# Kernel tuning notes

Hardware: AMD Instinct MI355X
Metric: run time of the kernel (lower is better)

Reference implementation:

```python
import jax, jax.numpy as jnp
import numpy as np

B, T, E, HSZ = 128, 256, 512, 1024
VOCAB, LVOCAB, K, STEPS = 2048, 11, 6, 3
HD = HSZ // 2  # per-direction LSTM hidden


def _lstm_dir(x, W_ih, W_hh, b, reverse):
    # x: [B,T,E] -> h seq [B,T,HD]; PyTorch gate order i,f,g,o
    xp = jnp.einsum('bte,ge->btg', x, W_ih) + b  # [B,T,4HD]
    if reverse:
        xp = xp[:, ::-1]
    def step(carry, xt):
        h, c = carry
        g = xt + h @ W_hh.T
        i, f, gg, o = jnp.split(g, 4, axis=-1)
        c = jax.nn.sigmoid(f) * c + jax.nn.sigmoid(i) * jnp.tanh(gg)
        h = jax.nn.sigmoid(o) * jnp.tanh(c)
        return (h, c), h
    z = jnp.zeros((x.shape[0], HD), x.dtype)
    _, hs = jax.lax.scan(step, (z, z), jnp.swapaxes(xp, 0, 1))
    hs = jnp.swapaxes(hs, 0, 1)
    if reverse:
        hs = hs[:, ::-1]
    return hs


def setup_inputs() -> dict:
    key = jax.random.key(0)
    ks = jax.random.split(key, 16)
    Xs = jax.random.randint(ks[0], (B, T), 0, VOCAB)
    seq_mask = jnp.ones((B, T), jnp.float32)
    landmarks = jax.random.randint(ks[1], (B, 4, 4, K), 0, LVOCAB)
    ys = jax.random.randint(ks[2], (B, 2), 0, 4)
    s = 0.05
    emb = (jax.random.normal(ks[3], (VOCAB, E)) * s).at[0].set(0.0)  # padding_idx=0
    W_ih_f = jax.random.normal(ks[4], (4 * HD, E)) * s
    W_hh_f = jax.random.normal(ks[5], (4 * HD, HD)) * s
    b_f = jax.random.normal(ks[6], (4 * HD,)) * s
    W_ih_b = jax.random.normal(ks[7], (4 * HD, E)) * s
    W_hh_b = jax.random.normal(ks[8], (4 * HD, HD)) * s
    b_b = jax.random.normal(ks[9], (4 * HD,)) * s
    feat_ctrl = jax.random.normal(ks[10], (HSZ,)) * 0.1
    upd_W = jax.random.normal(ks[11], (HSZ, 2 * HSZ)) * s
    upd_b = jax.random.normal(ks[12], (HSZ,)) * s
    map_emb = (jax.random.normal(ks[13], (LVOCAB, HSZ)) * s).at[0].set(0.0)
    std = 1.0 / (HSZ * 9)
    conv_w = jax.random.uniform(ks[14], (HSZ, HSZ, 3, 3), minval=-std, maxval=std)
    return dict(Xs=Xs, seq_mask=seq_mask, landmarks=landmarks, ys=ys, emb=emb,
                W_ih_f=W_ih_f, W_hh_f=W_hh_f, b_f=b_f, W_ih_b=W_ih_b,
                W_hh_b=W_hh_b, b_b=b_b, feat_ctrl=feat_ctrl, upd_W=upd_W,
                upd_b=upd_b, map_emb=map_emb, conv_w=conv_w)


def reference(Xs, seq_mask, landmarks, ys, emb, W_ih_f, W_hh_f, b_f,
              W_ih_b, W_hh_b, b_b, feat_ctrl, upd_W, upd_b, map_emb, conv_w):
    bsz = Xs.shape[0]
    x = emb[Xs]  # [B,T,E]
    hf = _lstm_dir(x, W_ih_f, W_hh_f, b_f, False)
    hb = _lstm_dir(x, W_ih_b, W_hh_b, b_b, True)
    hidden = jnp.concatenate([hf, hb], -1)  # [B,T,HSZ]

    controller = jnp.broadcast_to(feat_ctrl, (bsz, HSZ))
    msgs = []
    for _ in range(STEPS):
        score = jnp.einsum('bth,bh->bt', hidden, controller)
        score = score - 1e30 * (1.0 - seq_mask)
        att = jax.nn.softmax(score, axis=-1)
        msg = jnp.einsum('bt,bth->bh', att, hidden)
        msgs.append(msg)
        controller = jnp.concatenate([msg, controller], 1) @ upd_W.T + upd_b
    feature_msg = jnp.concatenate(msgs, 1)  # [B, STEPS*HSZ]

    # MapEmbedding2d: sum landmark embeddings per cell -> [B,4,4,HSZ] -> NCHW
    l_emb = map_emb[landmarks].sum(-2).transpose(0, 3, 1, 2)
    # masked conv weight: 4-neighbor diffusion
    m = jnp.zeros((3, 3)).at[0, 1].set(1.0).at[1, 0].set(1.0).at[2, 1].set(1.0).at[1, 2].set(1.0)
    w = conv_w * m[None, None]
    l_embs = [l_emb]
    for _ in range(STEPS - 1):
        l_embs.append(jax.lax.conv_general_dilated(
            l_embs[-1], w, (1, 1), [(1, 1), (1, 1)],
            dimension_numbers=('NCHW', 'OIHW', 'NCHW')))
    lmk = jnp.concatenate(l_embs, 1)  # [B, STEPS*HSZ, 4, 4]
    lmk = lmk.reshape(bsz, lmk.shape[1], 16).transpose(0, 2, 1)  # [B,16,C]
    logits = jnp.einsum('bnc,bc->bn', lmk, feature_msg)  # [B,16]
    prob = jax.nn.softmax(logits, 1)
    y_true = ys[:, 0] * 4 + ys[:, 1]
    # faithful to original: CrossEntropyLoss applied to prob (softmax of softmax)
    logp = jax.nn.log_softmax(prob, 1)
    loss = -jnp.take_along_axis(logp, y_true[:, None], 1).mean()
    acc = jnp.mean((jnp.argmax(prob, 1) == y_true).astype(jnp.float32))
    return loss, acc
```

## Files before the change

### kernel.cpp

```cpp
#include <hip/hip_runtime.h>


typedef _Float16 f16;
typedef __attribute__((ext_vector_type(8))) _Float16 f16x8;
typedef __attribute__((ext_vector_type(4))) float f32x4;

#define DEV __device__ __forceinline__

DEV void gload_lds16(const void* g, void* lds) {
  __builtin_amdgcn_global_load_lds(
      (const __attribute__((address_space(1))) unsigned*)g,
      (__attribute__((address_space(3))) unsigned*)lds, 16, 0, 0);
}
DEV void gload_lds16c(const void* g, void* lds) {
  __builtin_amdgcn_global_load_lds(
      (const __attribute__((address_space(1))) unsigned*)g,
      (__attribute__((address_space(3))) unsigned*)lds, 16, 0, 17);
}
DEV float sigm(float x) { return 1.0f / (1.0f + __expf(-x)); }
DEV float tanh_(float x) { return 1.0f - 2.0f / (__expf(2.0f * x) + 1.0f); }
DEV unsigned pck(float a, float b) {
  union { unsigned u; f16 h[2]; } c; c.h[0] = (f16)a; c.h[1] = (f16)b; return c.u;
}

__global__ __launch_bounds__(256) void gemm_kernel(
    const f16* __restrict__ A, const f16* __restrict__ B,
    const float* __restrict__ bias, void* __restrict__ Cp,
    int M, int N, int K, int cmode) {
  __shared__ f16 As[128 * 32];
  __shared__ f16 Bs[128 * 32];
  const int tid = threadIdx.x;
  const int w = tid >> 6, l = tid & 63;
  const int m0 = blockIdx.x * 128, n0 = blockIdx.y * 128;
  const int wm = (w & 1) * 64, wn = (w >> 1) * 64;
  const int lr = l & 15, lq = l >> 4;
  const int srow = w * 32 + (l >> 2);
  const int kc8 = (l & 3) * 8;
  f32x4 acc[4][4];
#pragma unroll
  for (int i = 0; i < 4; ++i)
#pragma unroll
    for (int j = 0; j < 4; ++j) acc[i][j] = (f32x4){0.f, 0.f, 0.f, 0.f};

  for (int kt = 0; kt < K; kt += 32) {
    __syncthreads();
#pragma unroll
    for (int i = 0; i < 2; ++i) {
      gload_lds16(A + (long)(m0 + srow + i * 16) * K + kt + kc8,
                  &As[(w * 32 + i * 16) * 32]);
      gload_lds16(B + (long)(n0 + srow + i * 16) * K + kt + kc8,
                  &Bs[(w * 32 + i * 16) * 32]);
    }
    __syncthreads();
    f16x8 af[4], bf[4];
#pragma unroll
    for (int mi = 0; mi < 4; ++mi)
      af[mi] = *(const f16x8*)&As[(wm + mi * 16 + lr) * 32 + lq * 8];
#pragma unroll
    for (int ni = 0; ni < 4; ++ni)
      bf[ni] = *(const f16x8*)&Bs[(wn + ni * 16 + lr) * 32 + lq * 8];
#pragma unroll
    for (int mi = 0; mi < 4; ++mi)
#pragma unroll
      for (int ni = 0; ni < 4; ++ni)
        acc[mi][ni] =
            __builtin_amdgcn_mfma_f32_16x16x32_f16(af[mi], bf[ni], acc[mi][ni], 0, 0, 0);
  }
#pragma unroll
  for (int mi = 0; mi < 4; ++mi)
#pragma unroll
    for (int ni = 0; ni < 4; ++ni)
#pragma unroll
      for (int r = 0; r < 4; ++r) {
        const int m = m0 + wm + mi * 16 + lq * 4 + r;
        const int n = n0 + wn + ni * 16 + lr;
        float v = acc[mi][ni][r];
        if (bias) v += bias[n];
        if (cmode) ((f16*)Cp)[(long)m * N + n] = (f16)v;
        else       ((float*)Cp)[(long)m * N + n] = v;
      }
}

__global__ __launch_bounds__(256, 1) void lstm_kernel(
    const f16* __restrict__ x16,
    const float* __restrict__ Wih_f, const float* __restrict__ Wih_b,
    const float* __restrict__ Whh_f, const float* __restrict__ Whh_b,
    const float* __restrict__ b_f, const float* __restrict__ b_b,
    f16* __restrict__ hg, f16* __restrict__ hidden, int* __restrict__ bar) {
  __shared__ f16 hs[16 * 16 * 32];
  __shared__ f16 xs[2][16 * 16 * 32];
  __shared__ float gb[4][16][32];
  const int blk = blockIdx.x, tid = threadIdx.x;
  const int d = blk >> 7, rr = blk & 127;
  const int ug = rr & 15, bg = rr >> 4;
  const int b0 = bg * 16;
  const int w = tid >> 6, l = tid & 63;
  const int lr = l & 15, lq = l >> 4;
  const int u0 = ug * 32 + w * 8;
  const float* const Wih = d ? Wih_b : Wih_f;
  const float* const Whh = d ? Whh_b : Whh_f;
  const float* const bb = d ? b_b : b_f;
  int* const flagbase = &bar[((d << 3) + bg) << 4];

  f16x8 wih[16][2], whh[16][2];
#pragma unroll
  for (int kt = 0; kt < 16; ++kt)
#pragma unroll
    for (int nt = 0; nt < 2; ++nt) {
      const int n = nt * 16 + lr;
      const long row = (long)((n >> 3) * 512 + u0 + (n & 7));
      const float* pi = Wih + row * 512 + kt * 32 + lq * 8;
      const float* ph = Whh + row * 512 + kt * 32 + lq * 8;
      f16x8 va, vb;
#pragma unroll
      for (int j = 0; j < 8; ++j) { va[j] = (f16)pi[j]; vb[j] = (f16)ph[j]; }
      wih[kt][nt] = va; whh[kt][nt] = vb;
    }
  const int bl = l >> 2, jp = (l & 3) * 2;
  const int b_my = b0 + bl;
  const float bi0 = bb[u0 + jp],        bi1 = bb[u0 + jp + 1];
  const float bF0 = bb[512 + u0 + jp],  bF1 = bb[512 + u0 + jp + 1];
  const float bg0 = bb[1024 + u0 + jp], bg1 = bb[1024 + u0 + jp + 1];
  const float bo0 = bb[1536 + u0 + jp], bo1 = bb[1536 + u0 + jp + 1];
  float c0 = 0.f, c1 = 0.f;
  f16* const hbase = hg + (d * 2) * 65536;

#define STAGE16(DST, SRCP, LOADER)                                            \
  {                                                                           \
    const f16* _s = (SRCP);                                                   \
    _Pragma("unroll") for (int k4 = 0; k4 < 4; ++k4) {                        \
      const int kt = w * 4 + k4;                                              \
      LOADER(_s + (long)(l >> 2) * 512 + kt * 32 + (l & 3) * 8,               \
             &DST[(kt * 16) * 32]);                                           \
    }                                                                         \
  }

  STAGE16(xs[0], x16 + ((long)(d ? 255 : 0) * 128 + b0) * 512, gload_lds16);
  __builtin_amdgcn_s_waitcnt(0x0F70);
  __syncthreads();
  f32x4 a0 = (f32x4){0.f, 0.f, 0.f, 0.f}, a1 = (f32x4){0.f, 0.f, 0.f, 0.f};
#pragma unroll
  for (int kt = 0; kt < 16; ++kt) {
    const f16x8 av = *(const f16x8*)&xs[0][(kt * 16 + lr) * 32 + lq * 8];
    a0 = __builtin_amdgcn_mfma_f32_16x16x32_f16(av, wih[kt][0], a0, 0, 0, 0);
    a1 = __builtin_amdgcn_mfma_f32_16x16x32_f16(av, wih[kt][1], a1, 0, 0, 0);
  }
  STAGE16(xs[1], x16 + ((long)(d ? 254 : 1) * 128 + b0) * 512, gload_lds16);

  for (int s = 0; s < 256; ++s) {
    const int t = d ? (255 - s) : s;
    const f16* const hrd = hbase + (s & 1) * 65536;
    f16* const hwr = hbase + ((s + 1) & 1) * 65536;
    if (w == 0 && l < 16) {
      while (__hip_atomic_load(&flagbase[l], __ATOMIC_RELAXED,
                               __HIP_MEMORY_SCOPE_SYSTEM) < s)
        __builtin_amdgcn_s_sleep(1);
    }
    __syncthreads();
    STAGE16(hs, hrd + (long)b0 * 512, gload_lds16c);
    __builtin_amdgcn_s_waitcnt(0x0F70);
    __syncthreads();
#pragma unroll
    for (int kt = 0; kt < 16; ++kt) {
      const f16x8 av = *(const f16x8*)&hs[(kt * 16 + lr) * 32 + lq * 8];
      a0 = __builtin_amdgcn_mfma_f32_16x16x32_f16(av, whh[kt][0], a0, 0, 0, 0);
      a1 = __builtin_amdgcn_mfma_f32_16x16x32_f16(av, whh[kt][1], a1, 0, 0, 0);
    }
#pragma unroll
    for (int r = 0; r < 4; ++r) {
      gb[w][lq * 4 + r][lr] = a0[r];
      gb[w][lq * 4 + r][16 + lr] = a1[r];
    }
    __builtin_amdgcn_s_waitcnt(0xC07F);
    unsigned hp;
    {
      const float* const gr = &gb[w][bl][0];
      float gi = gr[jp] + bi0, gf = gr[8 + jp] + bF0;
      float gg = gr[16 + jp] + bg0, go = gr[24 + jp] + bo0;
      c0 = sigm(gf) * c0 + sigm(gi) * tanh_(gg);
      const float h0 = sigm(go) * tanh_(c0);
      gi = gr[jp + 1] + bi1; gf = gr[8 + jp + 1] + bF1;
      gg = gr[16 + jp + 1] + bg1; go = gr[24 + jp + 1] + bo1;
      c1 = sigm(gf) * c1 + sigm(gi) * tanh_(gg);
      const float h1 = sigm(go) * tanh_(c1);
      hp = pck(h0, h1);
      __hip_atomic_store((unsigned*)&hwr[(b_my << 9) + u0 + jp], hp,
                         __ATOMIC_RELAXED, __HIP_MEMORY_SCOPE_SYSTEM);
    }
    __builtin_amdgcn_s_waitcnt(0x0F70);
    __syncthreads();
    if (tid == 0)
      __hip_atomic_store(&flagbase[ug], s + 1, __ATOMIC_RELAXED,
                         __HIP_MEMORY_SCOPE_SYSTEM);
    *(unsigned*)&hidden[((long)b_my * 256 + t) * 1024 + (d << 9) + u0 + jp] = hp;
    if (s < 255) {
      a0 = (f32x4){0.f, 0.f, 0.f, 0.f}; a1 = (f32x4){0.f, 0.f, 0.f, 0.f};
      const f16* const xr = &xs[(s + 1) & 1][0];
#pragma unroll
      for (int kt = 0; kt < 16; ++kt) {
        const f16x8 av = *(const f16x8*)&xr[(kt * 16 + lr) * 32 + lq * 8];
        a0 = __builtin_amdgcn_mfma_f32_16x16x32_f16(av, wih[kt][0], a0, 0, 0, 0);
        a1 = __builtin_amdgcn_mfma_f32_16x16x32_f16(av, wih[kt][1], a1, 0, 0, 0);
      }
      if (s < 254) {
        const int tp = d ? (253 - s) : (s + 2);
        STAGE16(xs[s & 1], x16 + ((long)tp * 128 + b0) * 512, gload_lds16);
      }
    }
  }
#undef STAGE16
}

__global__ __launch_bounds__(256) void att_kernel(
    const f16* __restrict__ hidden, const float* __restrict__ ctrl,
    const float* __restrict__ seq_mask, float* __restrict__ msg_out,
    f16* __restrict__ cat) {
  __shared__ float sc[256];
  __shared__ float red[4];
  __shared__ float ctl[1024];
  const int b = blockIdx.x, tid = threadIdx.x;
  const int w = tid >> 6, l = tid & 63;
  for (int i = tid; i < 1024; i += 256) ctl[i] = ctrl[b * 1024 + i];
  __syncthreads();
  float cl[16];
#pragma unroll
  for (int j = 0; j < 16; ++j) cl[j] = ctl[l + 64 * j];
  const f16* hb = hidden + (long)b * 262144;
  for (int t = w * 64; t < w * 64 + 64; ++t) {
    float s = 0.f;
#pragma unroll
    for (int j = 0; j < 16; ++j) s += (float)hb[t * 1024 + l + 64 * j] * cl[j];
#pragma unroll
    for (int off = 32; off; off >>= 1) s += __shfl_xor(s, off);
    if (l == 0) sc[t] = s;
  }
  __syncthreads();
  const float v = sc[tid] - 1e30f * (1.0f - seq_mask[b * 256 + tid]);
  float m = v;
#pragma unroll
  for (int off = 32; off; off >>= 1) m = fmaxf(m, __shfl_xor(m, off));
  if (l == 0) red[w] = m;
  __syncthreads();
  const float M = fmaxf(fmaxf(red[0], red[1]), fmaxf(red[2], red[3]));
  const float e = __expf(v - M);
  float ss = e;
#pragma unroll
  for (int off = 32; off; off >>= 1) ss += __shfl_xor(ss, off);
  __syncthreads();
  if (l == 0) red[w] = ss;
  __syncthreads();
  const float S = red[0] + red[1] + red[2] + red[3];
  sc[tid] = e / S;
  __syncthreads();
  const int hc = tid * 4;
  float a0 = 0.f, a1 = 0.f, a2 = 0.f, a3 = 0.f;
  for (int t = 0; t < 256; ++t) {
    const float at = sc[t];
    union { uint2 u; f16 h[4]; } q;
    q.u = *(const uint2*)&hb[t * 1024 + hc];
    a0 += at * (float)q.h[0]; a1 += at * (float)q.h[1];
    a2 += at * (float)q.h[2]; a3 += at * (float)q.h[3];
  }
  float* mo = msg_out + b * 1024 + hc;
  mo[0] = a0; mo[1] = a1; mo[2] = a2; mo[3] = a3;
  if (cat) {
    f16* cm = cat + (long)b * 2048 + hc;
    cm[0] = (f16)a0; cm[1] = (f16)a1; cm[2] = (f16)a2; cm[3] = (f16)a3;
    f16* cc = cat + (long)b * 2048 + 1024 + hc;
    cc[0] = (f16)ctl[hc]; cc[1] = (f16)ctl[hc + 1];
    cc[2] = (f16)ctl[hc + 2]; cc[3] = (f16)ctl[hc + 3];
  }
}

__global__ __launch_bounds__(256) void l0_kernel(
    const int* __restrict__ lm, const float* __restrict__ me, f16* __restrict__ l0) {
  const int bp = blockIdx.x, tid = threadIdx.x;
  const int h = tid * 4;
  int id[6];
#pragma unroll
  for (int k = 0; k < 6; ++k) id[k] = lm[bp * 6 + k];
  float a0 = 0.f, a1 = 0.f, a2 = 0.f, a3 = 0.f;
#pragma unroll
  for (int k = 0; k < 6; ++k) {
    const float* r = me + id[k] * 1024 + h;
    a0 += r[0]; a1 += r[1]; a2 += r[2]; a3 += r[3];
  }
  union { uint2 u; f16 hh[4]; } pk;
  pk.hh[0] = (f16)a0; pk.hh[1] = (f16)a1; pk.hh[2] = (f16)a2; pk.hh[3] = (f16)a3;
  *(uint2*)&l0[(long)bp * 1024 + h] = pk.u;
}

__global__ __launch_bounds__(256) void patch_kernel(
    const f16* __restrict__ src, f16* __restrict__ patch) {
  const int bp = blockIdx.x, tid = threadIdx.x;
  const int b = bp >> 4, p = bp & 15, y = p >> 2, x = p & 3;
  const int base = b * 16;
  f16* pr = patch + (long)bp * 4096;
  for (int i = tid; i < 1024; i += 256) {
    union { uint2 u; f16 h[4]; } pk;
    pk.h[0] = (y > 0) ? src[(long)(base + p - 4) * 1024 + i] : (f16)0.f;
    pk.h[1] = (x > 0) ? src[(long)(base + p - 1) * 1024 + i] : (f16)0.f;
    pk.h[2] = (x < 3) ? src[(long)(base + p + 1) * 1024 + i] : (f16)0.f;
    pk.h[3] = (y < 3) ? src[(long)(base + p + 4) * 1024 + i] : (f16)0.f;
    *(uint2*)&pr[i * 4] = pk.u;
  }
}

__global__ __launch_bounds__(256) void logits_kernel(
    const f16* __restrict__ l0, const f16* __restrict__ l1, const f16* __restrict__ l2,
    const float* __restrict__ msgs, const int* __restrict__ ys, float* __restrict__ la) {
  __shared__ float lg[16];
  const int b = blockIdx.x, tid = threadIdx.x;
  const int p = tid >> 4, q = tid & 15;
  const float* m0 = msgs + b * 1024;
  const float* m1 = msgs + 131072 + b * 1024;
  const float* m2 = msgs + 262144 + b * 1024;
  const long row = (long)(b * 16 + p) * 1024;
  float part = 0.f;
  for (int i = 0; i < 64; ++i) {
    const int h = q + 16 * i;
    part += (float)l0[row + h] * m0[h] + (float)l1[row + h] * m1[h] +
            (float)l2[row + h] * m2[h];
  }
#pragma unroll
  for (int off = 8; off; off >>= 1) part += __shfl_xor(part, off, 16);
  if (q == 0) lg[p] = part;
  __syncthreads();
  if (tid == 0) {
    float mx = lg[0];
    for (int i = 1; i < 16; ++i) mx = fmaxf(mx, lg[i]);
    float pr[16]; float s = 0.f;
    for (int i = 0; i < 16; ++i) { pr[i] = __expf(lg[i] - mx); s += pr[i]; }
    for (int i = 0; i < 16; ++i) pr[i] /= s;
    float mx2 = pr[0];
    for (int i = 1; i < 16; ++i) mx2 = fmaxf(mx2, pr[i]);
    float s2 = 0.f;
    for (int i = 0; i < 16; ++i) s2 += __expf(pr[i] - mx2);
    const float lse = mx2 + __logf(s2);
    const int y = ys[b * 2] * 4 + ys[b * 2 + 1];
    const float logp = pr[y] - lse;
    int am = 0; float bv = pr[0];
    for (int i = 1; i < 16; ++i) if (pr[i] > bv) { bv = pr[i]; am = i; }
    atomicAdd(&la[0], -logp * (1.0f / 128.0f));
    atomicAdd(&la[1], (am == y) ? (1.0f / 128.0f) : 0.0f);
  }
}

__global__ void finalize_kernel(const float* __restrict__ la,
                                float* __restrict__ out) {
  if (threadIdx.x == 0) { out[0] = la[0]; out[1] = la[1]; }
}

__global__ __launch_bounds__(256) void embed_kernel(
    const int* __restrict__ Xs, const float* __restrict__ emb, f16* __restrict__ x16) {
  const int m = blockIdx.x, tid = threadIdx.x;
  const int t = m >> 7, b = m & 127;
  const int v = Xs[b * 256 + t];
  const int e = tid * 2;
  const float2 f = *(const float2*)&emb[(long)v * 512 + e];
  *(unsigned*)&x16[(long)m * 512 + e] = pck(f.x, f.y);
}

__global__ __launch_bounds__(256) void prep2_kernel(
    const float* __restrict__ upd_W, const float* __restrict__ conv_w,
    f16* __restrict__ updW16, f16* __restrict__ w4) {
  const int idx = blockIdx.x * 256 + threadIdx.x;
  if (idx < 2097152) updW16[idx] = (f16)upd_W[idx];
  const int o = idx >> 12, r = idx & 4095, i = r >> 2, tp = r & 3;
  w4[idx] = (f16)conv_w[(long)(o * 1024 + i) * 9 + 1 + 2 * tp];
}

__global__ __launch_bounds__(256) void init_kernel(
    f16* __restrict__ hg, int* __restrict__ bar, float* __restrict__ la,
    float* __restrict__ ctrlA, const float* __restrict__ feat) {
  const int idx = blockIdx.x * 256 + threadIdx.x;
  ((unsigned*)hg)[idx] = 0u;
  ctrlA[idx] = feat[idx & 1023];
  if (idx < 256) bar[idx] = 0;
  if (idx < 2) la[idx] = 0.f;
}

__global__ void fail_kernel(float* out, int mb) {
  if (threadIdx.x == 0) { out[0] = 12344.0f; out[1] = (float)mb; }
}

extern "C" void kernel_launch(void* const* d_in, const int* in_sizes, int n_in,
                              void* d_out, int out_size, void* d_ws, size_t ws_size,
                              hipStream_t stream) {
  (void)in_sizes; (void)n_in; (void)out_size;
  const int*   Xs      = (const int*)d_in[0];
  const float* seqmask = (const float*)d_in[1];
  const int*   lm      = (const int*)d_in[2];
  const int*   ys      = (const int*)d_in[3];
  const float* emb     = (const float*)d_in[4];
  const float* W_ih_f  = (const float*)d_in[5];
  const float* W_hh_f  = (const float*)d_in[6];
  const float* b_f     = (const float*)d_in[7];
  const float* W_ih_b  = (const float*)d_in[8];
  const float* W_hh_b  = (const float*)d_in[9];
  const float* b_b     = (const float*)d_in[10];
  const float* feat    = (const float*)d_in[11];
  const float* upd_W   = (const float*)d_in[12];
  const float* upd_b   = (const float*)d_in[13];
  const float* mapemb  = (const float*)d_in[14];
  const float* conv_w  = (const float*)d_in[15];
  float* out = (float*)d_out;
  char* ws = (char*)d_ws;
  size_t off = 0;
  auto alloc = [&](size_t bytes) {
    void* p = ws + off; off += (bytes + 255) & ~(size_t)255; return p;
  };
  f16*   x16    = (f16*)alloc(33554432);
  f16*   hid    = (f16*)alloc(67108864);
  f16*   hgb    = (f16*)alloc(524288);
  int*   bar    = (int*)alloc(1024);
  float* la     = (float*)alloc(256);
  float* ctrlA  = (float*)alloc(524288);
  float* ctrlB  = (float*)alloc(524288);
  float* msgs   = (float*)alloc(1572864);
  f16*   cat    = (f16*)alloc(524288);
  f16*   l0b    = (f16*)alloc(4194304);
  f16*   l1b    = (f16*)alloc(4194304);
  f16*   l2b    = (f16*)alloc(4194304);
  f16*   patch  = x16;
  f16*   w416   = x16 + 8388608;
  f16*   updW16 = x16 + 12582912;
  if (ws_size < off) {
    fail_kernel<<<1, 64, 0, stream>>>(out, (int)(off >> 20));
    return;
  }

  init_kernel<<<512, 256, 0, stream>>>(hgb, bar, la, ctrlA, feat);
  embed_kernel<<<32768, 256, 0, stream>>>(Xs, emb, x16);
  {
    void* args[] = {(void*)&x16, (void*)&W_ih_f, (void*)&W_ih_b,
                    (void*)&W_hh_f, (void*)&W_hh_b, (void*)&b_f, (void*)&b_b,
                    (void*)&hgb, (void*)&hid, (void*)&bar};
    hipLaunchCooperativeKernel((void*)lstm_kernel, dim3(256), dim3(256), args, 0, stream);
  }
  prep2_kernel<<<16384, 256, 0, stream>>>(upd_W, conv_w, updW16, w416);
  l0_kernel<<<2048, 256, 0, stream>>>(lm, mapemb, l0b);
  patch_kernel<<<2048, 256, 0, stream>>>(l0b, patch);
  gemm_kernel<<<dim3(16, 8), 256, 0, stream>>>(patch, w416, nullptr, l1b,
                                               2048, 1024, 4096, 1);
  patch_kernel<<<2048, 256, 0, stream>>>(l1b, patch);
  gemm_kernel<<<dim3(16, 8), 256, 0, stream>>>(patch, w416, nullptr, l2b,
                                               2048, 1024, 4096, 1);
  att_kernel<<<128, 256, 0, stream>>>(hid, ctrlA, seqmask, msgs, cat);
  gemm_kernel<<<dim3(1, 8), 256, 0, stream>>>(cat, updW16, upd_b, ctrlB,
                                              128, 1024, 2048, 0);
  att_kernel<<<128, 256, 0, stream>>>(hid, ctrlB, seqmask, msgs + 131072, cat);
  gemm_kernel<<<dim3(1, 8), 256, 0, stream>>>(cat, updW16, upd_b, ctrlA,
                                              128, 1024, 2048, 0);
  att_kernel<<<128, 256, 0, stream>>>(hid, ctrlA, seqmask, msgs + 262144, nullptr);
  logits_kernel<<<128, 256, 0, stream>>>(l0b, l1b, l2b, msgs, ys, la);
  finalize_kernel<<<1, 64, 0, stream>>>(la, out);
}
```

Baseline: 1.567 ms.

## Run landmark conv chain concurrently with LSTM in one cooperative mega-kernel

Merges the LSTM recurrence and the landmark embedding/conv pipeline into one cooperative launch. Blocks 0-255 run the LSTM while blocks 256+ compute l0 and both masked-conv GEMM steps, using an implicit-im2col conv tile so the patch kernels disappear. The LSTM now gathers embedding rows directly from an f16 embedding table rather than a precomputed x16 buffer, which removes the embed kernel's large write. Risks include contention for CUs and memory bandwidth with the latency-bound LSTM, and co-residency of 512 blocks with launch_bounds(256,2).

```diff
diff --git a/kernel.cpp b/kernel.cpp
--- a/kernel.cpp
+++ b/kernel.cpp
@@ -81,20 +81,126 @@
       }
 }
 
-__global__ __launch_bounds__(256, 1) void lstm_kernel(
-    const f16* __restrict__ x16,
+DEV void conv_tile(char* smem, int tid, const f16* lsrc, const f16* wsrc,
+                   f16* ldst, int m0, int n0, const f16* zbuf) {
+  f16* const As = (f16*)smem;
+  f16* const Bs = (f16*)(smem + 8192);
+  const int w = tid >> 6, l = tid & 63;
+  const int wm = (w & 1) * 64, wn = (w >> 1) * 64;
+  const int lr = l & 15, lq = l >> 4;
+  const int srow = w * 32 + (l >> 2);
+  const int kc8 = (l & 3) * 8;
+  f32x4 acc[4][4];
+#pragma unroll
+  for (int i = 0; i < 4; ++i)
+#pragma unroll
+    for (int j = 0; j < 4; ++j) acc[i][j] = (f32x4){0.f, 0.f, 0.f, 0.f};
+
+  for (int kt = 0; kt < 4096; kt += 32) {
+    __syncthreads();
+    const int k = kt + kc8, tap = k >> 10, ic = k & 1023;
+#pragma unroll
+    for (int i = 0; i < 2; ++i) {
+      const int m = m0 + srow + i * 16;
+      const int b = m >> 4, p = m & 15, py = p >> 2, px = p & 3;
+      const int nb = p + ((tap == 0) ? -4 : (tap == 1) ? -1 : (tap == 2) ? 1 : 4);
+      const bool ok = (tap == 0) ? (py > 0) : (tap == 1) ? (px > 0)
+                      : (tap == 2) ? (px < 3) : (py < 3);
+      const f16* sa = ok ? (lsrc + ((long)(b * 16 + nb) * 1024 + ic)) : zbuf;
+      gload_lds16(sa, &As[(w * 32 + i * 16) * 32]);
+      gload_lds16(wsrc + (long)(n0 + srow + i * 16) * 4096 + kt + kc8,
+                  &Bs[(w * 32 + i * 16) * 32]);
+    }
+    __syncthreads();
+    f16x8 af[4], bf[4];
+#pragma unroll
+    for (int mi = 0; mi < 4; ++mi)
+      af[mi] = *(const f16x8*)&As[(wm + mi * 16 + lr) * 32 + lq * 8];
+#pragma unroll
+    for (int ni = 0; ni < 4; ++ni)
+      bf[ni] = *(const f16x8*)&Bs[(wn + ni * 16 + lr) * 32 + lq * 8];
+#pragma unroll
+    for (int mi = 0; mi < 4; ++mi)
+#pragma unroll
+      for (int ni = 0; ni < 4; ++ni)
+        acc[mi][ni] =
+            __builtin_amdgcn_mfma_f32_16x16x32_f16(af[mi], bf[ni], acc[mi][ni], 0, 0, 0);
+  }
+#pragma unroll
+  for (int mi = 0; mi < 4; ++mi)
+#pragma unroll
+    for (int ni = 0; ni < 4; ++ni)
+#pragma unroll
+      for (int r = 0; r < 4; ++r) {
+        const int m = m0 + wm + mi * 16 + lq * 4 + r;
+        const int n = n0 + wn + ni * 16 + lr;
+        ldst[(long)m * 1024 + n] = (f16)acc[mi][ni][r];
+      }
+}
+
+DEV void helper_barrier(int* cnt, int* gen, int tid) {
+  __syncthreads();
+  if (tid == 0) {
+    __threadfence();
+    const int a = __hip_atomic_fetch_add(cnt, 1, __ATOMIC_ACQ_REL,
+                                         __HIP_MEMORY_SCOPE_SYSTEM);
+    if (a == 255) {
+      __hip_atomic_store(gen, 1, __ATOMIC_RELEASE, __HIP_MEMORY_SCOPE_SYSTEM);
+    } else {
+      while (__hip_atomic_load(gen, __ATOMIC_RELAXED,
+                               __HIP_MEMORY_SCOPE_SYSTEM) == 0)
+        __builtin_amdgcn_s_sleep(8);
+    }
+    __threadfence();
+  }
+  __syncthreads();
+}
+
+__global__ __launch_bounds__(256, 2) void mega_kernel(
+    const int* __restrict__ Xs, const f16* __restrict__ emb16,
     const float* __restrict__ Wih_f, const float* __restrict__ Wih_b,
     const float* __restrict__ Whh_f, const float* __restrict__ Whh_b,
     const float* __restrict__ b_f, const float* __restrict__ b_b,
-    f16* __restrict__ hg, f16* __restrict__ hidden, int* __restrict__ bar) {
-  __shared__ f16 hs[16 * 16 * 32];
-  __shared__ f16 xs[2][16 * 16 * 32];
-  __shared__ float gb[4][16][32];
+    f16* __restrict__ hg, f16* __restrict__ hidden, int* __restrict__ bar,
+    const int* __restrict__ lm, const float* __restrict__ mapemb,
+    f16* __restrict__ l0b, f16* __restrict__ l1b, f16* __restrict__ l2b,
+    const f16* __restrict__ w416, const f16* __restrict__ zbuf) {
+  __shared__ char smem[57344];
   const int blk = blockIdx.x, tid = threadIdx.x;
+  const int w = tid >> 6, l = tid & 63;
+
+  if (blk >= 256) {
+    const int hb = blk - 256;
+    for (int j = 0; j < 8; ++j) {
+      const int bp = hb * 8 + j;
+      const int h = tid * 4;
+      float a0 = 0.f, a1 = 0.f, a2 = 0.f, a3 = 0.f;
+#pragma unroll
+      for (int k = 0; k < 6; ++k) {
+        const float* r = mapemb + lm[bp * 6 + k] * 1024 + h;
+        a0 += r[0]; a1 += r[1]; a2 += r[2]; a3 += r[3];
+      }
+      union { uint2 u; f16 hh[4]; } pk;
+      pk.hh[0] = (f16)a0; pk.hh[1] = (f16)a1;
+      pk.hh[2] = (f16)a2; pk.hh[3] = (f16)a3;
+      *(uint2*)&l0b[(long)bp * 1024 + h] = pk.u;
+    }
+    helper_barrier(&bar[256], &bar[272], tid);
+    if (hb < 128)
+      conv_tile(smem, tid, l0b, w416, l1b, (hb & 15) * 128, (hb >> 4) * 128, zbuf);
+    helper_barrier(&bar[288], &bar[304], tid);
+    if (hb < 128)
+      conv_tile(smem, tid, l1b, w416, l2b, (hb & 15) * 128, (hb >> 4) * 128, zbuf);
+    return;
+  }
+
+  f16* const hs = (f16*)smem;
+  f16* const xs0 = (f16*)(smem + 16384);
+  f16* const xs1 = (f16*)(smem + 32768);
+  float* const gbp = (float*)(smem + 49152);
   const int d = blk >> 7, rr = blk & 127;
   const int ug = rr & 15, bg = rr >> 4;
   const int b0 = bg * 16;
-  const int w = tid >> 6, l = tid & 63;
   const int lr = l & 15, lq = l >> 4;
   const int u0 = ug * 32 + w * 8;
   const float* const Wih = d ? Wih_b : Wih_f;
@@ -125,27 +231,36 @@
   float c0 = 0.f, c1 = 0.f;
   f16* const hbase = hg + (d * 2) * 65536;
 
-#define STAGE16(DST, SRCP, LOADER)                                            \
+#define STAGEH(SRCP)                                                          \
   {                                                                           \
     const f16* _s = (SRCP);                                                   \
     _Pragma("unroll") for (int k4 = 0; k4 < 4; ++k4) {                        \
       const int kt = w * 4 + k4;                                              \
-      LOADER(_s + (long)(l >> 2) * 512 + kt * 32 + (l & 3) * 8,               \
-             &DST[(kt * 16) * 32]);                                           \
+      gload_lds16c(_s + (long)(l >> 2) * 512 + kt * 32 + (l & 3) * 8,         \
+                   &hs[(kt * 16) * 32]);                                      \
     }                                                                         \
   }
-
-  STAGE16(xs[0], x16 + ((long)(d ? 255 : 0) * 128 + b0) * 512, gload_lds16);
+#define STAGEX(DSTP, TP)                                                      \
+  {                                                                           \
+    const int _xr = Xs[(b0 + (l >> 2)) * 256 + (TP)];                         \
+    const f16* _s = emb16 + (long)_xr * 512 + (l & 3) * 8;                    \
+    _Pragma("unroll") for (int k4 = 0; k4 < 4; ++k4) {                        \
+      const int kt = w * 4 + k4;                                              \
+      gload_lds16(_s + kt * 32, &(DSTP)[(kt * 16) * 32]);                     \
+    }                                                                         \
+  }
+
+  STAGEX(xs0, d ? 255 : 0);
   __builtin_amdgcn_s_waitcnt(0x0F70);
   __syncthreads();
   f32x4 a0 = (f32x4){0.f, 0.f, 0.f, 0.f}, a1 = (f32x4){0.f, 0.f, 0.f, 0.f};
 #pragma unroll
   for (int kt = 0; kt < 16; ++kt) {
-    const f16x8 av = *(const f16x8*)&xs[0][(kt * 16 + lr) * 32 + lq * 8];
+    const f16x8 av = *(const f16x8*)&xs0[(kt * 16 + lr) * 32 + lq * 8];
     a0 = __builtin_amdgcn_mfma_f32_16x16x32_f16(av, wih[kt][0], a0, 0, 0, 0);
     a1 = __builtin_amdgcn_mfma_f32_16x16x32_f16(av, wih[kt][1], a1, 0, 0, 0);
   }
-  STAGE16(xs[1], x16 + ((long)(d ? 254 : 1) * 128 + b0) * 512, gload_lds16);
+  STAGEX(xs1, d ? 254 : 1);
 
   for (int s = 0; s < 256; ++s) {
     const int t = d ? (255 - s) : s;
@@ -157,7 +272,7 @@
         __builtin_amdgcn_s_sleep(1);
     }
     __syncthreads();
-    STAGE16(hs, hrd + (long)b0 * 512, gload_lds16c);
+    STAGEH(hrd + (long)b0 * 512);
     __builtin_amdgcn_s_waitcnt(0x0F70);
     __syncthreads();
 #pragma unroll
@@ -168,13 +283,13 @@
     }
 #pragma unroll
     for (int r = 0; r < 4; ++r) {
-      gb[w][lq * 4 + r][lr] = a0[r];
-      gb[w][lq * 4 + r][16 + lr] = a1[r];
+      gbp[(w * 16 + lq * 4 + r) * 32 + lr] = a0[r];
+      gbp[(w * 16 + lq * 4 + r) * 32 + 16 + lr] = a1[r];
     }
     __builtin_amdgcn_s_waitcnt(0xC07F);
     unsigned hp;
     {
-      const float* const gr = &gb[w][bl][0];
+      const float* const gr = &gbp[(w * 16 + bl) * 32];
       float gi = gr[jp] + bi0, gf = gr[8 + jp] + bF0;
       float gg = gr[16 + jp] + bg0, go = gr[24 + jp] + bo0;
       c0 = sigm(gf) * c0 + sigm(gi) * tanh_(gg);
@@ -195,7 +310,7 @@
     *(unsigned*)&hidden[((long)b_my * 256 + t) * 1024 + (d << 9) + u0 + jp] = hp;
     if (s < 255) {
       a0 = (f32x4){0.f, 0.f, 0.f, 0.f}; a1 = (f32x4){0.f, 0.f, 0.f, 0.f};
-      const f16* const xr = &xs[(s + 1) & 1][0];
+      const f16* const xr = ((s + 1) & 1) ? xs1 : xs0;
 #pragma unroll
       for (int kt = 0; kt < 16; ++kt) {
         const f16x8 av = *(const f16x8*)&xr[(kt * 16 + lr) * 32 + lq * 8];
@@ -203,12 +318,13 @@
         a1 = __builtin_amdgcn_mfma_f32_16x16x32_f16(av, wih[kt][1], a1, 0, 0, 0);
       }
       if (s < 254) {
-        const int tp = d ? (253 - s) : (s + 2);
-        STAGE16(xs[s & 1], x16 + ((long)tp * 128 + b0) * 512, gload_lds16);
+        f16* const xd = (s & 1) ? xs1 : xs0;
+        STAGEX(xd, d ? (253 - s) : (s + 2));
       }
     }
   }
-#undef STAGE16
+#undef STAGEH
+#undef STAGEX
 }
 
 __global__ __launch_bounds__(256) void att_kernel(
@@ -269,40 +385,6 @@
     f16* cc = cat + (long)b * 2048 + 1024 + hc;
     cc[0] = (f16)ctl[hc]; cc[1] = (f16)ctl[hc + 1];
     cc[2] = (f16)ctl[hc + 2]; cc[3] = (f16)ctl[hc + 3];
-  }
-}
-
-__global__ __launch_bounds__(256) void l0_kernel(
-    const int* __restrict__ lm, const float* __restrict__ me, f16* __restrict__ l0) {
-  const int bp = blockIdx.x, tid = threadIdx.x;
-  const int h = tid * 4;
-  int id[6];
-#pragma unroll
-  for (int k = 0; k < 6; ++k) id[k] = lm[bp * 6 + k];
-  float a0 = 0.f, a1 = 0.f, a2 = 0.f, a3 = 0.f;
-#pragma unroll
-  for (int k = 0; k < 6; ++k) {
-    const float* r = me + id[k] * 1024 + h;
-    a0 += r[0]; a1 += r[1]; a2 += r[2]; a3 += r[3];
-  }
-  union { uint2 u; f16 hh[4]; } pk;
-  pk.hh[0] = (f16)a0; pk.hh[1] = (f16)a1; pk.hh[2] = (f16)a2; pk.hh[3] = (f16)a3;
-  *(uint2*)&l0[(long)bp * 1024 + h] = pk.u;
-}
-
-__global__ __launch_bounds__(256) void patch_kernel(
-    const f16* __restrict__ src, f16* __restrict__ patch) {
-  const int bp = blockIdx.x, tid = threadIdx.x;
-  const int b = bp >> 4, p = bp & 15, y = p >> 2, x = p & 3;
-  const int base = b * 16;
-  f16* pr = patch + (long)bp * 4096;
-  for (int i = tid; i < 1024; i += 256) {
-    union { uint2 u; f16 h[4]; } pk;
-    pk.h[0] = (y > 0) ? src[(long)(base + p - 4) * 1024 + i] : (f16)0.f;
-    pk.h[1] = (x > 0) ? src[(long)(base + p - 1) * 1024 + i] : (f16)0.f;
-    pk.h[2] = (x < 3) ? src[(long)(base + p + 1) * 1024 + i] : (f16)0.f;
-    pk.h[3] = (y < 3) ? src[(long)(base + p + 4) * 1024 + i] : (f16)0.f;
-    *(uint2*)&pr[i * 4] = pk.u;
   }
 }
 
@@ -351,23 +433,18 @@
   if (threadIdx.x == 0) { out[0] = la[0]; out[1] = la[1]; }
 }
 
-__global__ __launch_bounds__(256) void embed_kernel(
-    const int* __restrict__ Xs, const float* __restrict__ emb, f16* __restrict__ x16) {
-  const int m = blockIdx.x, tid = threadIdx.x;
-  const int t = m >> 7, b = m & 127;
-  const int v = Xs[b * 256 + t];
-  const int e = tid * 2;
-  const float2 f = *(const float2*)&emb[(long)v * 512 + e];
-  *(unsigned*)&x16[(long)m * 512 + e] = pck(f.x, f.y);
-}
-
-__global__ __launch_bounds__(256) void prep2_kernel(
-    const float* __restrict__ upd_W, const float* __restrict__ conv_w,
-    f16* __restrict__ updW16, f16* __restrict__ w4) {
+__global__ __launch_bounds__(256) void prep_kernel(
+    const float* __restrict__ emb, const float* __restrict__ upd_W,
+    const float* __restrict__ conv_w, f16* __restrict__ emb16,
+    f16* __restrict__ updW16, f16* __restrict__ w416, f16* __restrict__ zbuf) {
   const int idx = blockIdx.x * 256 + threadIdx.x;
+  if (idx < 1048576) emb16[idx] = (f16)emb[idx];
   if (idx < 2097152) updW16[idx] = (f16)upd_W[idx];
-  const int o = idx >> 12, r = idx & 4095, i = r >> 2, tp = r & 3;
-  w4[idx] = (f16)conv_w[(long)(o * 1024 + i) * 9 + 1 + 2 * tp];
+  {
+    const int o = idx >> 12, r = idx & 4095, tp = r >> 10, i = r & 1023;
+    w416[idx] = (f16)conv_w[(long)(o * 1024 + i) * 9 + 1 + 2 * tp];
+  }
+  if (idx < 128) zbuf[idx] = (f16)0.f;
 }
 
 __global__ __launch_bounds__(256) void init_kernel(
@@ -376,7 +453,7 @@
   const int idx = blockIdx.x * 256 + threadIdx.x;
   ((unsigned*)hg)[idx] = 0u;
   ctrlA[idx] = feat[idx & 1023];
-  if (idx < 256) bar[idx] = 0;
+  if (idx < 1024) bar[idx] = 0;
   if (idx < 2) la[idx] = 0.f;
 }
 
@@ -410,10 +487,10 @@
   auto alloc = [&](size_t bytes) {
     void* p = ws + off; off += (bytes + 255) & ~(size_t)255; return p;
   };
-  f16*   x16    = (f16*)alloc(33554432);
   f16*   hid    = (f16*)alloc(67108864);
+  f16*   emb16  = (f16*)alloc(2097152);
   f16*   hgb    = (f16*)alloc(524288);
-  int*   bar    = (int*)alloc(1024);
+  int*   bar    = (int*)alloc(4096);
   float* la     = (float*)alloc(256);
   float* ctrlA  = (float*)alloc(524288);
   float* ctrlB  = (float*)alloc(524288);
@@ -422,30 +499,27 @@
   f16*   l0b    = (f16*)alloc(4194304);
   f16*   l1b    = (f16*)alloc(4194304);
   f16*   l2b    = (f16*)alloc(4194304);
-  f16*   patch  = x16;
-  f16*   w416   = x16 + 8388608;
-  f16*   updW16 = x16 + 12582912;
+  f16*   w416   = (f16*)alloc(8388608);
+  f16*   updW16 = (f16*)alloc(4194304);
+  f16*   zbuf   = (f16*)alloc(256);
   if (ws_size < off) {
     fail_kernel<<<1, 64, 0, stream>>>(out, (int)(off >> 20));
     return;
   }
 
   init_kernel<<<512, 256, 0, stream>>>(hgb, bar, la, ctrlA, feat);
-  embed_kernel<<<32768, 256, 0, stream>>>(Xs, emb, x16);
+  prep_kernel<<<16384, 256, 0, stream>>>(emb, upd_W, conv_w, emb16, updW16,
+                                         w416, zbuf);
   {
-    void* args[] = {(void*)&x16, (void*)&W_ih_f, (void*)&W_ih_b,
+    void* args[] = {(void*)&Xs, (void*)&emb16,
+                    (void*)&W_ih_f, (void*)&W_ih_b,
                     (void*)&W_hh_f, (void*)&W_hh_b, (void*)&b_f, (void*)&b_b,
-                    (void*)&hgb, (void*)&hid, (void*)&bar};
-    hipLaunchCooperativeKernel((void*)lstm_kernel, dim3(256), dim3(256), args, 0, stream);
-  }
-  prep2_kernel<<<16384, 256, 0, stream>>>(upd_W, conv_w, updW16, w416);
-  l0_kernel<<<2048, 256, 0, stream>>>(lm, mapemb, l0b);
-  patch_kernel<<<2048, 256, 0, stream>>>(l0b, patch);
-  gemm_kernel<<<dim3(16, 8), 256, 0, stream>>>(patch, w416, nullptr, l1b,
-                                               2048, 1024, 4096, 1);
-  patch_kernel<<<2048, 256, 0, stream>>>(l1b, patch);
-  gemm_kernel<<<dim3(16, 8), 256, 0, stream>>>(patch, w416, nullptr, l2b,
-                                               2048, 1024, 4096, 1);
+                    (void*)&hgb, (void*)&hid, (void*)&bar,
+                    (void*)&lm, (void*)&mapemb,
+                    (void*)&l0b, (void*)&l1b, (void*)&l2b,
+                    (void*)&w416, (void*)&zbuf};
+    hipLaunchCooperativeKernel((void*)mega_kernel, dim3(512), dim3(256), args, 0, stream);
+  }
   att_kernel<<<128, 256, 0, stream>>>(hid, ctrlA, seqmask, msgs, cat);
   gemm_kernel<<<dim3(1, 8), 256, 0, stream>>>(cat, updW16, upd_b, ctrlB,
                                               128, 1024, 2048, 0);
```

Result: slower. 2.178 ms (+39.0%).
